# Performance work log

Measured on AMD Instinct MI355X. Metric: run time of the kernel, lower is better.

Reference implementation:

```python
import jax, jax.numpy as jnp
import numpy as np

N = 50000
E = 800000
F_IN = 128
HID = 64
NEG_SLOPE = 0.2
LN_EPS = 1e-5


def _gat_layer(x, W, att_src, att_dst, bias, src, dst, heads, out_ch, concat):
    # x: [N, in], W: [in, heads*out_ch], att_*: [heads, out_ch]
    n = x.shape[0]
    xp = (x @ W).reshape(n, heads, out_ch)                    # [N, H, C]
    a_src = jnp.einsum('nhc,hc->nh', xp, att_src)             # [N, H]
    a_dst = jnp.einsum('nhc,hc->nh', xp, att_dst)             # [N, H]
    e = jax.nn.leaky_relu(a_src[src] + a_dst[dst], NEG_SLOPE) # [E, H]
    # edge softmax over incoming edges of each destination node
    m = jax.ops.segment_max(e, dst, num_segments=n)           # [N, H]
    ex = jnp.exp(e - m[dst])
    s = jax.ops.segment_sum(ex, dst, num_segments=n)          # [N, H]
    alpha = ex / s[dst]                                       # [E, H]
    agg = jax.ops.segment_sum(xp[src] * alpha[:, :, None], dst, num_segments=n)
    out = agg.reshape(n, heads * out_ch) if concat else agg.mean(axis=1)
    return out + bias


def _layernorm(x, g, b):
    mu = x.mean(-1, keepdims=True)
    var = x.var(-1, keepdims=True)
    return (x - mu) / jnp.sqrt(var + LN_EPS) * g + b


def setup_inputs() -> dict:
    key = jax.random.key(0)
    ks = jax.random.split(key, 12)
    sc = 0.1
    return {
        'x': jax.random.normal(ks[0], (N, F_IN), jnp.float32),
        'edge_index': jax.random.randint(ks[1], (2, E), 0, N, jnp.int64),
        'W1': jax.random.normal(ks[2], (F_IN, 4 * HID), jnp.float32) * sc,
        'att_src1': jax.random.normal(ks[3], (4, HID), jnp.float32) * sc,
        'att_dst1': jax.random.normal(ks[4], (4, HID), jnp.float32) * sc,
        'b1': jnp.zeros((4 * HID,), jnp.float32),
        'ln1_g': jnp.ones((4 * HID,), jnp.float32),
        'ln1_b': jnp.zeros((4 * HID,), jnp.float32),
        'W2': jax.random.normal(ks[5], (4 * HID, 2 * HID), jnp.float32) * sc,
        'att_src2': jax.random.normal(ks[6], (2, HID), jnp.float32) * sc,
        'att_dst2': jax.random.normal(ks[7], (2, HID), jnp.float32) * sc,
        'b2': jnp.zeros((2 * HID,), jnp.float32),
        'ln2_g': jnp.ones((2 * HID,), jnp.float32),
        'ln2_b': jnp.zeros((2 * HID,), jnp.float32),
        'W3': jax.random.normal(ks[8], (2 * HID, F_IN), jnp.float32) * sc,
        'att_src3': jax.random.normal(ks[9], (1, F_IN), jnp.float32) * sc,
        'att_dst3': jax.random.normal(ks[10], (1, F_IN), jnp.float32) * sc,
        'b3': jnp.zeros((F_IN,), jnp.float32),
    }


def reference(x, edge_index, W1, att_src1, att_dst1, b1, ln1_g, ln1_b,
              W2, att_src2, att_dst2, b2, ln2_g, ln2_b,
              W3, att_src3, att_dst3, b3):
    n = x.shape[0]
    # PyG GATConv default: add self-loops
    loop = jnp.arange(n, dtype=edge_index.dtype)
    src = jnp.concatenate([edge_index[0], loop])
    dst = jnp.concatenate([edge_index[1], loop])

    h = _gat_layer(x, W1, att_src1, att_dst1, b1, src, dst, 4, HID, True)
    h = jax.nn.elu(_layernorm(h, ln1_g, ln1_b))
    # dropout p=0.2 is identity in eval mode
    h = _gat_layer(h, W2, att_src2, att_dst2, b2, src, dst, 2, HID, True)
    h = jax.nn.elu(_layernorm(h, ln2_g, ln2_b))
    out = _gat_layer(h, W3, att_src3, att_dst3, b3, src, dst, 1, F_IN, True)
    return out
```

## Files before the change

### kernel.cpp

```cpp
#include <hip/hip_runtime.h>
#include <hip/hip_bf16.h>
#include <hip/hip_fp16.h>
#include <math.h>

#define N_NODES 50000
#define N_EDGES 800000
#define E_TOT   850000
#define SCAN_B  1024

typedef __hip_bfloat16 bf16;
typedef __attribute__((ext_vector_type(8))) short short8v;
typedef __attribute__((ext_vector_type(4))) float float4v;

static __device__ __forceinline__ float u2f(unsigned short u) {
    return __uint_as_float(((unsigned int)u) << 16);
}
static __device__ __forceinline__ unsigned short f2u(float f) {
    unsigned int u = __float_as_uint(f);
    return (unsigned short)((u + 0x7FFFu + ((u >> 16) & 1u)) >> 16);
}
static __device__ __forceinline__ float ldr(const void* p, int i, bool bf) {
    return bf ? u2f(((const unsigned short*)p)[i]) : ((const float*)p)[i];
}

__global__ void k_init(const unsigned int* __restrict__ x32,
                       const unsigned int* __restrict__ ei32,
                       int* __restrict__ zero_base, int nzero,
                       int* __restrict__ flags) {
    int i = blockIdx.x * 256 + threadIdx.x;
    if (i < nzero) zero_base[i] = 0;
    if (blockIdx.x == 0) {
        __shared__ int c1, c2;
        if (threadIdx.x == 0) { c1 = 0; c2 = 0; }
        __syncthreads();
        unsigned int e = (x32[threadIdx.x] >> 7) & 0xFF;
        if (e >= 90 && e <= 140) atomicAdd(&c1, 1);
        if (threadIdx.x < 64 && ei32[2 * threadIdx.x + 1] == 0) atomicAdd(&c2, 1);
        __syncthreads();
        if (threadIdx.x == 0) {
            flags[0] = (c1 >= 128) ? 1 : 0;
            flags[1] = (c2 >= 48) ? 1 : 0;
        }
    }
}

__global__ void k_hist(const int* __restrict__ flags, const void* __restrict__ ei,
                       int* __restrict__ counts) {
    int i = blockIdx.x * blockDim.x + threadIdx.x;
    if (i >= E_TOT) return;
    int d;
    if (i < N_EDGES)
        d = flags[1] ? (int)((const long long*)ei)[N_EDGES + i]
                     : ((const int*)ei)[N_EDGES + i];
    else
        d = i - N_EDGES;
    atomicAdd(&counts[d], 1);
}

__global__ void k_scan1(const int* __restrict__ counts, int* __restrict__ scanned,
                        int* __restrict__ partial, int n) {
    __shared__ int sh[SCAN_B];
    int i = blockIdx.x * SCAN_B + threadIdx.x;
    sh[threadIdx.x] = (i < n) ? counts[i] : 0;
    __syncthreads();
    for (int off = 1; off < SCAN_B; off <<= 1) {
        int t = (threadIdx.x >= off) ? sh[threadIdx.x - off] : 0;
        __syncthreads();
        sh[threadIdx.x] += t;
        __syncthreads();
    }
    if (i < n) scanned[i] = sh[threadIdx.x];
    if (threadIdx.x == SCAN_B - 1) partial[blockIdx.x] = sh[SCAN_B - 1];
}

__global__ void k_scan2(int* __restrict__ partial, int nb) {
    if (threadIdx.x == 0 && blockIdx.x == 0) {
        int acc = 0;
        for (int b = 0; b < nb; b++) { int t = partial[b]; partial[b] = acc; acc += t; }
    }
}

__global__ void k_scan3(const int* __restrict__ counts, const int* __restrict__ scanned,
                        const int* __restrict__ partial, int* __restrict__ rowptr,
                        int* __restrict__ cursor, int n) {
    int i = blockIdx.x * blockDim.x + threadIdx.x;
    if (i >= n) return;
    int incl = scanned[i] + partial[i / SCAN_B];
    rowptr[i + 1] = incl;
    cursor[i]     = incl - counts[i];
    if (i == 0) rowptr[0] = 0;
}

__global__ void k_scatter(const int* __restrict__ flags, const void* __restrict__ ei,
                          int* __restrict__ cursor, int* __restrict__ csr_src) {
    int i = blockIdx.x * blockDim.x + threadIdx.x;
    if (i >= E_TOT) return;
    int s, d;
    if (i < N_EDGES) {
        if (flags[1]) {
            s = (int)((const long long*)ei)[i];
            d = (int)((const long long*)ei)[N_EDGES + i];
        } else {
            s = ((const int*)ei)[i];
            d = ((const int*)ei)[N_EDGES + i];
        }
    } else {
        s = d = i - N_EDGES;
    }
    int pos = atomicAdd(&cursor[d], 1);
    csr_src[pos] = s;
}

__global__ void k_prepx(const int* __restrict__ flags, const void* __restrict__ x,
                        bf16* __restrict__ xb, int n4) {
    int i = blockIdx.x * blockDim.x + threadIdx.x;
    if (i >= n4) return;
    if (flags[0]) {
        ((ushort4*)xb)[i] = ((const ushort4*)x)[i];
    } else {
        float4 f = ((const float4*)x)[i];
        ushort4 u;
        u.x = f2u(f.x); u.y = f2u(f.y); u.z = f2u(f.z); u.w = f2u(f.w);
        ((ushort4*)xb)[i] = u;
    }
}

struct PrepArgs { const void* src[13]; int off[13]; int len[13]; };

__global__ void k_prep_misc(const int* __restrict__ flags,
                            const void* __restrict__ W1, const void* __restrict__ W2,
                            const void* __restrict__ W3,
                            bf16* __restrict__ Wt1, bf16* __restrict__ Wt2,
                            bf16* __restrict__ Wt3,
                            PrepArgs a, float* __restrict__ par) {
    const bool bf = flags[0] != 0;
    const int b = blockIdx.x;
    if (b < 320) {
        int i = b * 256 + threadIdx.x;
        if (i < 32768) {
            int k = i >> 8, c = i & 255;
            Wt1[c * 128 + k] = __float2bfloat16(ldr(W1, i, bf));
        } else if (i < 65536) {
            int j = i - 32768, k = j >> 7, c = j & 127;
            Wt2[c * 256 + k] = __float2bfloat16(ldr(W2, j, bf));
        } else if (i < 81920) {
            int j = i - 65536, k = j >> 7, c = j & 127;
            Wt3[c * 128 + k] = __float2bfloat16(ldr(W3, j, bf));
        }
    } else {
        int seg = b - 320;
        for (int i = threadIdx.x; i < a.len[seg]; i += blockDim.x)
            par[a.off[seg] + i] = ldr(a.src[seg], i, bf);
    }
}

template<int K, int NT, int SPW, int H>
__global__ __launch_bounds__(256) void k_gemm_mfma2(const bf16* __restrict__ A,
                                                    const bf16* __restrict__ Wt,
                                                    unsigned short* __restrict__ xp,
                                                    const float* __restrict__ att_s,
                                                    const float* __restrict__ att_d,
                                                    float* __restrict__ asr,
                                                    float* __restrict__ adst) {
    constexpr int KF     = K / 32;
    constexpr int NSG    = NT / (16 * SPW);
    constexpr int NTILES = N_NODES / 16;
    constexpr int C      = NT / H;
    const int l    = threadIdx.x & 63;
    const int wid  = blockIdx.x * 4 + (threadIdx.x >> 6);
    const int sg   = wid % NSG;
    const int wpg  = (gridDim.x * 4) / NSG;
    const int t0   = wid / NSG;
    const int r16  = l & 15;
    const int kgrp = (l >> 4) * 8;
    const int head = (sg * SPW * 16) / C;

    short8v b[SPW][KF];
    float as_r[SPW][4], ad_r[SPW][4];
    #pragma unroll
    for (int s = 0; s < SPW; s++) {
        const int cs  = (sg * SPW + s) * 16;
        const int col = cs + r16;
        #pragma unroll
        for (int kf = 0; kf < KF; kf++)
            b[s][kf] = *(const short8v*)(Wt + (size_t)col * K + kf * 32 + kgrp);
        #pragma unroll
        for (int r = 0; r < 4; r++) {
            const int ch = cs + (l >> 4) * 4 + r;
            as_r[s][r] = att_s[ch];
            ad_r[s][r] = att_d[ch];
        }
    }

    for (int t = t0; t < NTILES; t += wpg) {
        const int m0 = t * 16;
        short8v a[KF];
        #pragma unroll
        for (int kf = 0; kf < KF; kf++)
            a[kf] = *(const short8v*)(A + (size_t)(m0 + r16) * K + kf * 32 + kgrp);
        float4v acc[SPW] = {};
        #pragma unroll
        for (int kf = 0; kf < KF; kf++)
            #pragma unroll
            for (int s = 0; s < SPW; s++)
                acc[s] = __builtin_amdgcn_mfma_f32_16x16x32_bf16(b[s][kf], a[kf], acc[s], 0, 0, 0);

        float pa = 0.f, pd = 0.f;
        #pragma unroll
        for (int s = 0; s < SPW; s++)
            #pragma unroll
            for (int r = 0; r < 4; r++) {
                pa = fmaf(acc[s][r], as_r[s][r], pa);
                pd = fmaf(acc[s][r], ad_r[s][r], pd);
            }
        pa += __shfl_xor(pa, 16); pa += __shfl_xor(pa, 32);
        pd += __shfl_xor(pd, 16); pd += __shfl_xor(pd, 32);
        if (l < 16) {
            atomicAdd(&asr [(size_t)(m0 + l) * H + head], pa);
            atomicAdd(&adst[(size_t)(m0 + l) * H + head], pd);
        }

        const int node = m0 + r16;
        #pragma unroll
        for (int s = 0; s < SPW; s++) {
            const int ch = (sg * SPW + s) * 16 + (l >> 4) * 4;
            uint2 o;
            o.x = (unsigned int)__half_as_ushort(__float2half(acc[s][0])) |
                  ((unsigned int)__half_as_ushort(__float2half(acc[s][1])) << 16);
            o.y = (unsigned int)__half_as_ushort(__float2half(acc[s][2])) |
                  ((unsigned int)__half_as_ushort(__float2half(acc[s][3])) << 16);
            *(uint2*)(xp + (size_t)node * NT + ch) = o;
        }
    }
}

template<int CT, int H, bool LAST>
__global__ __launch_bounds__(256) void k_agg8(const int* __restrict__ flags,
                                              const unsigned short* __restrict__ xp,
                                              const float* __restrict__ asr,
                                              const float* __restrict__ adst,
                                              const int* __restrict__ rowptr,
                                              const int* __restrict__ csr_src,
                                              const float* __restrict__ bias,
                                              const float* __restrict__ gamma,
                                              const float* __restrict__ beta,
                                              void* __restrict__ outv) {
    constexpr int V   = CT / 64;
    constexpr int C   = CT / H;
    constexpr int LPH = C / V;
    constexpr int ND  = V / 2;
    constexpr int STR = CT / 2;
    constexpr int G   = (ND == 2) ? 4 : 8;
    const int l     = threadIdx.x & 63;
    const int w     = threadIdx.x >> 6;
    const int hd    = l / LPH;
    const int slot  = l & (LPH - 1);
    const int lbase = hd * LPH;
    const unsigned int coff = ND * l;

    float bv[V], gv[V], bev[V];
    #pragma unroll
    for (int v = 0; v < V; v++) bv[v] = bias[V * l + v];
    if constexpr (!LAST) {
        #pragma unroll
        for (int v = 0; v < V; v++) {
            gv[v]  = gamma[V * l + v];
            bev[v] = beta [V * l + v];
        }
    }
    const unsigned int* xpd = (const unsigned int*)xp;

    const int n = blockIdx.x * 4 + w;
    if (n >= N_NODES) return;
    const int b0 = rowptr[n], b1 = rowptr[n + 1];
    const int deg = b1 - b0;
    const float ad = adst[n * H + hd];
    const int sn_first = csr_src[b0];

    float ssum = 0.f;
    float acc[V];
    #pragma unroll
    for (int v = 0; v < V; v++) acc[v] = 0.f;

    for (int cbase = 0; cbase < deg; cbase += LPH) {
        const int nn = min(LPH, deg - cbase);
        int   sn_l = sn_first;
        float p_l  = 0.f;
        if (slot < nn) {
            sn_l = csr_src[b0 + cbase + slot];
            float e = asr[(unsigned)(sn_l * H + hd)] + ad;
            e = e > 0.f ? e : 0.2f * e;
            p_l = __expf(fminf(e, 80.f));
        }
        const int nnG = (nn + G - 1) & ~(G - 1);
        for (int eb = 0; eb < nnG; eb += G) {
            unsigned int offs[G]; float ps[G];
            #pragma unroll
            for (int g = 0; g < G; g++) {
                int sn = __shfl(sn_l, lbase + eb + g);
                ps[g]  = __shfl(p_l,  lbase + eb + g);
                offs[g] = (unsigned int)sn * STR + coff;
            }
            unsigned int d[G][ND];
            #pragma unroll
            for (int g = 0; g < G; g++) {
                if constexpr (ND == 2)
                    *(uint2*)d[g] = *(const uint2*)(xpd + offs[g]);
                else
                    d[g][0] = xpd[offs[g]];
            }
            #pragma unroll
            for (int g = 0; g < G; g++) {
                ssum += ps[g];
                #pragma unroll
                for (int k = 0; k < ND; k++) {
                    __half2 h2 = *(__half2*)&d[g][k];
                    acc[2 * k]     = fmaf(ps[g], __low2float(h2),  acc[2 * k]);
                    acc[2 * k + 1] = fmaf(ps[g], __high2float(h2), acc[2 * k + 1]);
                }
            }
        }
    }
    const float inv_s = 1.f / ssum;
    #pragma unroll
    for (int v = 0; v < V; v++) acc[v] = fmaf(acc[v], inv_s, bv[v]);

    if constexpr (!LAST) {
        float lsum = 0.f, lsq = 0.f;
        #pragma unroll
        for (int v = 0; v < V; v++) { lsum += acc[v]; lsq = fmaf(acc[v], acc[v], lsq); }
        #pragma unroll
        for (int off = 1; off < 64; off <<= 1) {
            lsum += __shfl_xor(lsum, off);
            lsq  += __shfl_xor(lsq,  off);
        }
        float mu  = lsum * (1.f / CT);
        float var = lsq  * (1.f / CT) - mu * mu;
        float rs  = rsqrtf(var + 1e-5f);
        unsigned int od[ND];
        #pragma unroll
        for (int k = 0; k < ND; k++) {
            float y0 = (acc[2 * k]     - mu) * rs * gv[2 * k]     + bev[2 * k];
            float y1 = (acc[2 * k + 1] - mu) * rs * gv[2 * k + 1] + bev[2 * k + 1];
            y0 = y0 > 0.f ? y0 : expm1f(y0);
            y1 = y1 > 0.f ? y1 : expm1f(y1);
            od[k] = (unsigned int)f2u(y0) | ((unsigned int)f2u(y1) << 16);
        }
        unsigned int* ob = (unsigned int*)outv + (size_t)n * STR + coff;
        if constexpr (ND == 2) *(uint2*)ob = make_uint2(od[0], od[1]);
        else                   *ob = od[0];
    } else {
        if (flags[0]) {
            unsigned int o = (unsigned int)f2u(acc[0]) | ((unsigned int)f2u(acc[1]) << 16);
            *((unsigned int*)outv + (size_t)n * STR + coff) = o;
        } else {
            *(float2*)((float*)outv + (size_t)n * CT + V * l) = make_float2(acc[0], acc[1]);
        }
    }
}

extern "C" void kernel_launch(void* const* d_in, const int* in_sizes, int n_in,
                              void* d_out, int out_size, void* d_ws, size_t ws_size,
                              hipStream_t stream) {
    const void* x  = d_in[0];
    const void* ei = d_in[1];

    char* ws = (char*)d_ws;
    unsigned short* xp = (unsigned short*)(ws);
    bf16*  hbuf   = (bf16*)(ws + 25600000);
    int*   counts = (int*)  (ws + 51200000);
    float* asr1   = (float*)(ws + 51404096);
    float* adst1  = (float*)(ws + 52204096);
    float* asr2   = (float*)(ws + 53004096);
    float* adst2  = (float*)(ws + 53404096);
    float* asr3   = (float*)(ws + 53804096);
    float* adst3  = (float*)(ws + 54004096);
    const int kZeroInts = (54204096 - 51200000) / 4;
    int*   scannd = (int*)  (ws + 54204096);
    int*   part   = (int*)  (ws + 54404096);
    int*   rowptr = (int*)  (ws + 54404352);
    int*   cursor = (int*)  (ws + 54604416);
    int*   csrsrc = (int*)  (ws + 54804416);
    int*   flags  = (int*)  (ws + 58404416);
    bf16*  Wt1    = (bf16*) (ws + 58404480);
    bf16*  Wt2    = (bf16*) (ws + 58470016);
    bf16*  Wt3    = (bf16*) (ws + 58535552);
    float* params = (float*)(ws + 58568320);

    bf16* xb = hbuf;

    const int nb_scan = (N_NODES + SCAN_B - 1) / SCAN_B;
    const int AGGB    = (N_NODES + 3) / 4;

    k_init<<<(kZeroInts + 255) / 256, 256, 0, stream>>>((const unsigned int*)x,
                                                        (const unsigned int*)ei,
                                                        counts, kZeroInts, flags);

    k_hist  <<<(E_TOT + 255) / 256, 256, 0, stream>>>(flags, ei, counts);
    k_scan1 <<<nb_scan, SCAN_B, 0, stream>>>(counts, scannd, part, N_NODES);
    k_scan2 <<<1, 64, 0, stream>>>(part, nb_scan);
    k_scan3 <<<(N_NODES + 255) / 256, 256, 0, stream>>>(counts, scannd, part, rowptr, cursor, N_NODES);
    k_scatter<<<(E_TOT + 255) / 256, 256, 0, stream>>>(flags, ei, cursor, csrsrc);

    const int n4 = N_NODES * 128 / 4;
    k_prepx<<<(n4 + 255) / 256, 256, 0, stream>>>(flags, x, xb, n4);

    PrepArgs pa;
    const int srcs[13] = {3, 4, 5, 6, 7, 9, 10, 11, 12, 13, 15, 16, 17};
    const int offs[13] = {0, 256, 512, 768, 1024, 1280, 1408, 1536, 1664, 1792, 1920, 2048, 2176};
    const int lens[13] = {256, 256, 256, 256, 256, 128, 128, 128, 128, 128, 128, 128, 128};
    for (int i = 0; i < 13; i++) { pa.src[i] = d_in[srcs[i]]; pa.off[i] = offs[i]; pa.len[i] = lens[i]; }
    k_prep_misc<<<333, 256, 0, stream>>>(flags, d_in[2], d_in[8], d_in[14], Wt1, Wt2, Wt3, pa, params);

    k_gemm_mfma2<128, 256, 4, 4><<<768, 256, 0, stream>>>(xb, Wt1, xp, params + 0, params + 256, asr1, adst1);
    k_agg8<256, 4, false><<<AGGB, 256, 0, stream>>>(flags, xp, asr1, adst1, rowptr, csrsrc,
                                                    params + 512, params + 768, params + 1024, hbuf);

    k_gemm_mfma2<256, 128, 2, 2><<<768, 256, 0, stream>>>(hbuf, Wt2, xp, params + 1280, params + 1408, asr2, adst2);
    k_agg8<128, 2, false><<<AGGB, 256, 0, stream>>>(flags, xp, asr2, adst2, rowptr, csrsrc,
                                                    params + 1536, params + 1664, params + 1792, hbuf);

    k_gemm_mfma2<128, 128, 2, 1><<<768, 256, 0, stream>>>(hbuf, Wt3, xp, params + 1920, params + 2048, asr3, adst3);
    k_agg8<128, 1, true><<<AGGB, 256, 0, stream>>>(flags, xp, asr3, adst3, rowptr, csrsrc,
                                                   params + 2176, nullptr, nullptr, d_out);
}
```

Before: 307.8 us.

## Fold scan2 and prepx into neighbors, drop redundant atomics, split agg loop

Several independent changes. The single-thread scan2 kernel is removed, and each scan3 block now sums the preceding partials itself. The x-to-bf16 conversion is merged into the prep_misc launch. The GEMM writes attention logits with plain stores when each head is covered by one wave group, instead of using atomics. The aggregation loop is split into a full-chunk fast path with unrolled groups and a masked tail path. Together these cut kernel launches and branch overhead, at the cost of redundant serial partial sums in scan3.

```diff
diff --git a/kernel.cpp b/kernel.cpp
--- a/kernel.cpp
+++ b/kernel.cpp
@@ -73,19 +73,20 @@
     if (threadIdx.x == SCAN_B - 1) partial[blockIdx.x] = sh[SCAN_B - 1];
 }
 
-__global__ void k_scan2(int* __restrict__ partial, int nb) {
-    if (threadIdx.x == 0 && blockIdx.x == 0) {
-        int acc = 0;
-        for (int b = 0; b < nb; b++) { int t = partial[b]; partial[b] = acc; acc += t; }
-    }
-}
-
 __global__ void k_scan3(const int* __restrict__ counts, const int* __restrict__ scanned,
                         const int* __restrict__ partial, int* __restrict__ rowptr,
                         int* __restrict__ cursor, int n) {
-    int i = blockIdx.x * blockDim.x + threadIdx.x;
+    __shared__ int base_sh;
+    if (threadIdx.x == 0) {
+        const int jmax = (blockIdx.x * 256) / SCAN_B;
+        int acc = 0;
+        for (int b = 0; b < jmax; b++) acc += partial[b];
+        base_sh = acc;
+    }
+    __syncthreads();
+    int i = blockIdx.x * 256 + threadIdx.x;
     if (i >= n) return;
-    int incl = scanned[i] + partial[i / SCAN_B];
+    int incl = scanned[i] + base_sh;
     rowptr[i + 1] = incl;
     cursor[i]     = incl - counts[i];
     if (i == 0) rowptr[0] = 0;
@@ -111,23 +112,10 @@
     csr_src[pos] = s;
 }
 
-__global__ void k_prepx(const int* __restrict__ flags, const void* __restrict__ x,
-                        bf16* __restrict__ xb, int n4) {
-    int i = blockIdx.x * blockDim.x + threadIdx.x;
-    if (i >= n4) return;
-    if (flags[0]) {
-        ((ushort4*)xb)[i] = ((const ushort4*)x)[i];
-    } else {
-        float4 f = ((const float4*)x)[i];
-        ushort4 u;
-        u.x = f2u(f.x); u.y = f2u(f.y); u.z = f2u(f.z); u.w = f2u(f.w);
-        ((ushort4*)xb)[i] = u;
-    }
-}
-
 struct PrepArgs { const void* src[13]; int off[13]; int len[13]; };
 
 __global__ void k_prep_misc(const int* __restrict__ flags,
+                            const void* __restrict__ x, bf16* __restrict__ xb, int n4,
                             const void* __restrict__ W1, const void* __restrict__ W2,
                             const void* __restrict__ W3,
                             bf16* __restrict__ Wt1, bf16* __restrict__ Wt2,
@@ -147,10 +135,22 @@
             int j = i - 65536, k = j >> 7, c = j & 127;
             Wt3[c * 128 + k] = __float2bfloat16(ldr(W3, j, bf));
         }
-    } else {
+    } else if (b < 333) {
         int seg = b - 320;
         for (int i = threadIdx.x; i < a.len[seg]; i += blockDim.x)
             par[a.off[seg] + i] = ldr(a.src[seg], i, bf);
+    } else {
+        int i = (b - 333) * 256 + threadIdx.x;
+        if (i < n4) {
+            if (bf) {
+                ((ushort4*)xb)[i] = ((const ushort4*)x)[i];
+            } else {
+                float4 f = ((const float4*)x)[i];
+                ushort4 u;
+                u.x = f2u(f.x); u.y = f2u(f.y); u.z = f2u(f.z); u.w = f2u(f.w);
+                ((ushort4*)xb)[i] = u;
+            }
+        }
     }
 }
 
@@ -216,8 +216,13 @@
         pa += __shfl_xor(pa, 16); pa += __shfl_xor(pa, 32);
         pd += __shfl_xor(pd, 16); pd += __shfl_xor(pd, 32);
         if (l < 16) {
-            atomicAdd(&asr [(size_t)(m0 + l) * H + head], pa);
-            atomicAdd(&adst[(size_t)(m0 + l) * H + head], pd);
+            if constexpr (NSG == H) {
+                asr [(size_t)(m0 + l) * H + head] = pa;
+                adst[(size_t)(m0 + l) * H + head] = pd;
+            } else {
+                atomicAdd(&asr [(size_t)(m0 + l) * H + head], pa);
+                atomicAdd(&adst[(size_t)(m0 + l) * H + head], pd);
+            }
         }
 
         const int node = m0 + r16;
@@ -235,7 +240,7 @@
 }
 
 template<int CT, int H, bool LAST>
-__global__ __launch_bounds__(256) void k_agg8(const int* __restrict__ flags,
+__global__ __launch_bounds__(256) void k_agg9(const int* __restrict__ flags,
                                               const unsigned short* __restrict__ xp,
                                               const float* __restrict__ asr,
                                               const float* __restrict__ adst,
@@ -275,16 +280,53 @@
     const int b0 = rowptr[n], b1 = rowptr[n + 1];
     const int deg = b1 - b0;
     const float ad = adst[n * H + hd];
-    const int sn_first = csr_src[b0];
 
     float ssum = 0.f;
     float acc[V];
     #pragma unroll
     for (int v = 0; v < V; v++) acc[v] = 0.f;
 
-    for (int cbase = 0; cbase < deg; cbase += LPH) {
-        const int nn = min(LPH, deg - cbase);
-        int   sn_l = sn_first;
+    auto do_group = [&](int sn_l, float p_l, int eb) {
+        unsigned int offs[G]; float ps[G];
+        #pragma unroll
+        for (int g = 0; g < G; g++) {
+            int sn = __shfl(sn_l, lbase + eb + g);
+            ps[g]  = __shfl(p_l,  lbase + eb + g);
+            offs[g] = (unsigned int)sn * STR + coff;
+        }
+        unsigned int d[G][ND];
+        #pragma unroll
+        for (int g = 0; g < G; g++) {
+            if constexpr (ND == 2)
+                *(uint2*)d[g] = *(const uint2*)(xpd + offs[g]);
+            else
+                d[g][0] = xpd[offs[g]];
+        }
+        #pragma unroll
+        for (int g = 0; g < G; g++) {
+            ssum += ps[g];
+            #pragma unroll
+            for (int k = 0; k < ND; k++) {
+                __half2 h2 = *(__half2*)&d[g][k];
+                acc[2 * k]     = fmaf(ps[g], __low2float(h2),  acc[2 * k]);
+                acc[2 * k + 1] = fmaf(ps[g], __high2float(h2), acc[2 * k + 1]);
+            }
+        }
+    };
+
+    int cbase = 0;
+    for (; cbase + LPH <= deg; cbase += LPH) {
+        int sn_l = csr_src[b0 + cbase + slot];
+        float e = asr[(unsigned)(sn_l * H + hd)] + ad;
+        e = e > 0.f ? e : 0.2f * e;
+        float p_l = __expf(fminf(e, 80.f));
+        #pragma unroll
+        for (int eb = 0; eb < LPH; eb += G)
+            do_group(sn_l, p_l, eb);
+    }
+    if (cbase < deg) {
+        const int nn = deg - cbase;
+        int   sn_l = csr_src[b0];
         float p_l  = 0.f;
         if (slot < nn) {
             sn_l = csr_src[b0 + cbase + slot];
@@ -293,34 +335,10 @@
             p_l = __expf(fminf(e, 80.f));
         }
         const int nnG = (nn + G - 1) & ~(G - 1);
-        for (int eb = 0; eb < nnG; eb += G) {
-            unsigned int offs[G]; float ps[G];
-            #pragma unroll
-            for (int g = 0; g < G; g++) {
-                int sn = __shfl(sn_l, lbase + eb + g);
-                ps[g]  = __shfl(p_l,  lbase + eb + g);
-                offs[g] = (unsigned int)sn * STR + coff;
-            }
-            unsigned int d[G][ND];
-            #pragma unroll
-            for (int g = 0; g < G; g++) {
-                if constexpr (ND == 2)
-                    *(uint2*)d[g] = *(const uint2*)(xpd + offs[g]);
-                else
-                    d[g][0] = xpd[offs[g]];
-            }
-            #pragma unroll
-            for (int g = 0; g < G; g++) {
-                ssum += ps[g];
-                #pragma unroll
-                for (int k = 0; k < ND; k++) {
-                    __half2 h2 = *(__half2*)&d[g][k];
-                    acc[2 * k]     = fmaf(ps[g], __low2float(h2),  acc[2 * k]);
-                    acc[2 * k + 1] = fmaf(ps[g], __high2float(h2), acc[2 * k + 1]);
-                }
-            }
-        }
-    }
+        for (int eb = 0; eb < nnG; eb += G)
+            do_group(sn_l, p_l, eb);
+    }
+
     const float inv_s = 1.f / ssum;
     #pragma unroll
     for (int v = 0; v < V; v++) acc[v] = fmaf(acc[v], inv_s, bv[v]);
@@ -391,6 +409,7 @@
 
     const int nb_scan = (N_NODES + SCAN_B - 1) / SCAN_B;
     const int AGGB    = (N_NODES + 3) / 4;
+    const int n4      = N_NODES * 128 / 4;
 
     k_init<<<(kZeroInts + 255) / 256, 256, 0, stream>>>((const unsigned int*)x,
                                                         (const unsigned int*)ei,
@@ -398,29 +417,27 @@
 
     k_hist  <<<(E_TOT + 255) / 256, 256, 0, stream>>>(flags, ei, counts);
     k_scan1 <<<nb_scan, SCAN_B, 0, stream>>>(counts, scannd, part, N_NODES);
-    k_scan2 <<<1, 64, 0, stream>>>(part, nb_scan);
     k_scan3 <<<(N_NODES + 255) / 256, 256, 0, stream>>>(counts, scannd, part, rowptr, cursor, N_NODES);
     k_scatter<<<(E_TOT + 255) / 256, 256, 0, stream>>>(flags, ei, cursor, csrsrc);
-
-    const int n4 = N_NODES * 128 / 4;
-    k_prepx<<<(n4 + 255) / 256, 256, 0, stream>>>(flags, x, xb, n4);
 
     PrepArgs pa;
     const int srcs[13] = {3, 4, 5, 6, 7, 9, 10, 11, 12, 13, 15, 16, 17};
     const int offs[13] = {0, 256, 512, 768, 1024, 1280, 1408, 1536, 1664, 1792, 1920, 2048, 2176};
     const int lens[13] = {256, 256, 256, 256, 256, 128, 128, 128, 128, 128, 128, 128, 128};
     for (int i = 0; i < 13; i++) { pa.src[i] = d_in[srcs[i]]; pa.off[i] = offs[i]; pa.len[i] = lens[i]; }
-    k_prep_misc<<<333, 256, 0, stream>>>(flags, d_in[2], d_in[8], d_in[14], Wt1, Wt2, Wt3, pa, params);
+    k_prep_misc<<<333 + (n4 + 255) / 256, 256, 0, stream>>>(flags, x, xb, n4,
+                                                            d_in[2], d_in[8], d_in[14],
+                                                            Wt1, Wt2, Wt3, pa, params);
 
     k_gemm_mfma2<128, 256, 4, 4><<<768, 256, 0, stream>>>(xb, Wt1, xp, params + 0, params + 256, asr1, adst1);
-    k_agg8<256, 4, false><<<AGGB, 256, 0, stream>>>(flags, xp, asr1, adst1, rowptr, csrsrc,
+    k_agg9<256, 4, false><<<AGGB, 256, 0, stream>>>(flags, xp, asr1, adst1, rowptr, csrsrc,
                                                     params + 512, params + 768, params + 1024, hbuf);
 
     k_gemm_mfma2<256, 128, 2, 2><<<768, 256, 0, stream>>>(hbuf, Wt2, xp, params + 1280, params + 1408, asr2, adst2);
-    k_agg8<128, 2, false><<<AGGB, 256, 0, stream>>>(flags, xp, asr2, adst2, rowptr, csrsrc,
+    k_agg9<128, 2, false><<<AGGB, 256, 0, stream>>>(flags, xp, asr2, adst2, rowptr, csrsrc,
                                                     params + 1536, params + 1664, params + 1792, hbuf);
 
     k_gemm_mfma2<128, 128, 2, 1><<<768, 256, 0, stream>>>(hbuf, Wt3, xp, params + 1920, params + 2048, asr3, adst3);
-    k_agg8<128, 1, true><<<AGGB, 256, 0, stream>>>(flags, xp, asr3, adst3, rowptr, csrsrc,
+    k_agg9<128, 1, true><<<AGGB, 256, 0, stream>>>(flags, xp, asr3, adst3, rowptr, csrsrc,
                                                    params + 2176, nullptr, nullptr, d_out);
 }
```

Result: slower. 351.9 us (+14.3%).
